# Performance work log

Hardware: AMD Instinct MI355X
Metric: run time of the kernel (lower is better)

## Reference

```python
import jax, jax.numpy as jnp
import numpy as np

N = 100000   # nodes
E = 1600000  # edges
D = 128      # in_dim == hidden_dim (residual-friendly)
C = 47       # num_classes
EPS = 1e-5   # BatchNorm eps


def _glorot(key, shape):
    fan = shape[0] + shape[1]
    return jax.random.uniform(key, shape, jnp.float32, -1.0, 1.0) * np.sqrt(6.0 / fan)


def setup_inputs() -> dict:
    key = jax.random.key(0)
    ks = jax.random.split(key, 16)
    inp = {
        "x": jax.random.normal(ks[0], (N, D), jnp.float32),
        "edge_index": jax.random.randint(ks[1], (2, E), 0, N, jnp.int32),
    }
    # Per-layer SAGEConv params: lin_l (root, with bias) and lin_r (neighbor, no bias)
    for i, k in zip((1, 2, 3), (ks[2], ks[3], ks[4])):
        k1, k2 = jax.random.split(k)
        inp[f"Wl{i}"] = _glorot(k1, (D, D))
        inp[f"bl{i}"] = jnp.zeros((D,), jnp.float32)
        inp[f"Wr{i}"] = _glorot(k2, (D, D))
        inp[f"bn_g{i}"] = jnp.ones((D,), jnp.float32)
        inp[f"bn_b{i}"] = jnp.zeros((D,), jnp.float32)
    inp["lin_W"] = _glorot(ks[5], (C, D))
    inp["lin_b"] = jnp.zeros((C,), jnp.float32)
    return inp


def _sage_conv(x, src, dst, Wl, bl, Wr):
    # mean aggregation of source features at destination nodes
    msg = jax.ops.segment_sum(x[src], dst, num_segments=N)            # [N, D]
    cnt = jax.ops.segment_sum(jnp.ones((src.shape[0],), x.dtype), dst, num_segments=N)
    mean = msg / jnp.maximum(cnt, 1.0)[:, None]
    return x @ Wl.T + bl + mean @ Wr.T


def _batch_norm(h, g, b):
    mu = h.mean(axis=0)
    var = h.var(axis=0)
    return (h - mu) * jax.lax.rsqrt(var + EPS) * g + b


def reference(x, edge_index,
              Wl1, bl1, Wr1, bn_g1, bn_b1,
              Wl2, bl2, Wr2, bn_g2, bn_b2,
              Wl3, bl3, Wr3, bn_g3, bn_b3,
              lin_W, lin_b):
    src, dst = edge_index[0], edge_index[1]
    layers = [(Wl1, bl1, Wr1, bn_g1, bn_b1),
              (Wl2, bl2, Wr2, bn_g2, bn_b2),
              (Wl3, bl3, Wr3, bn_g3, bn_b3)]
    for Wl, bl, Wr, g, b in layers:
        h = _sage_conv(x, src, dst, Wl, bl, Wr)
        h = jax.nn.relu(_batch_norm(h, g, b))
        # dropout is identity in deterministic/eval reference
        x = x + h  # shapes always match since in_dim == hidden_dim
    return x @ lin_W.T + lin_b
```

## Files before the change

kernel.cpp:

```cpp
#include <hip/hip_runtime.h>

typedef __attribute__((ext_vector_type(8))) short short8;
typedef __attribute__((ext_vector_type(4))) float f32x4;
typedef __attribute__((ext_vector_type(2))) float f32x2;

constexpr int NN = 100000;
constexpr int EE = 1600000;
constexpr int DD = 128;
constexpr int CC = 47;
constexpr int NB = 391;
constexpr int BSLOT = 5120;
constexpr int GB = 782;

constexpr size_t OFF_XB   = 0;
constexpr size_t OFF_MB   = 25600000;
constexpr size_t OFF_HB   = 51200000;
constexpr size_t OFF_XQ   = 76800000;
constexpr size_t OFF_BIN  = 89600000;
constexpr size_t OFF_CSR  = 97607680;
constexpr size_t OFF_RP   = 104007680;
constexpr size_t OFF_CUR  = 104407808;
constexpr size_t OFF_BASE = 104409856;
constexpr size_t OFF_W    = 104411904;
constexpr size_t OFF_ST   = 104620800;
constexpr size_t OFF_PB   = 104621824;

static __device__ __forceinline__ float bf2f(unsigned short u) {
    return __uint_as_float(((unsigned)u) << 16);
}
static __device__ __forceinline__ unsigned short f2bf(float f) {
    unsigned u = __float_as_uint(f);
    unsigned r = (u + 0x7fffu + ((u >> 16) & 1u)) >> 16;
    return (unsigned short)r;
}
static __device__ __forceinline__ uint2 pack8_fp8(const float* f) {
    int w0 = 0, w1 = 0;
    w0 = __builtin_amdgcn_cvt_pk_fp8_f32(f[0], f[1], w0, false);
    w0 = __builtin_amdgcn_cvt_pk_fp8_f32(f[2], f[3], w0, true);
    w1 = __builtin_amdgcn_cvt_pk_fp8_f32(f[4], f[5], w1, false);
    w1 = __builtin_amdgcn_cvt_pk_fp8_f32(f[6], f[7], w1, true);
    return uint2{(unsigned)w0, (unsigned)w1};
}

__global__ void k_convw(const float* __restrict__ wl1, const float* __restrict__ wr1,
                        const float* __restrict__ wl2, const float* __restrict__ wr2,
                        const float* __restrict__ wl3, const float* __restrict__ wr3,
                        const float* __restrict__ lw, unsigned short* __restrict__ dst) {
    int id = blockIdx.x * 256 + threadIdx.x;
    if (id < 98304) {
        int L = id >> 15;
        int r = id & 32767;
        int mat = r >> 14;
        int t = r & 16383;
        int j = t & 7, lane = (t >> 3) & 63, ct = (t >> 9) & 7, ks = t >> 12;
        int row = ct * 16 + (lane & 15);
        int col = ks * 32 + ((lane >> 4) << 3) + j;
        const float* src = (L == 0) ? (mat ? wr1 : wl1)
                         : (L == 1) ? (mat ? wr2 : wl2)
                                    : (mat ? wr3 : wl3);
        dst[id] = f2bf(src[row * 128 + col]);
    } else if (id < 98304 + 6144) {
        int t = id - 98304;
        int j = t & 7, lane = (t >> 3) & 63, m = t >> 9;
        int ct = m % 3, ks = m / 3;
        int row = ct * 16 + (lane & 15);
        int col = ks * 32 + ((lane >> 4) << 3) + j;
        dst[id] = (row < CC) ? f2bf(lw[row * 128 + col]) : (unsigned short)0;
    }
}

__global__ void k_convx(const float* __restrict__ x, unsigned short* __restrict__ xb,
                        unsigned char* __restrict__ xq) {
    int i = (blockIdx.x * 256 + threadIdx.x) * 8;
    if (i >= NN * DD) return;
    float4 v1 = *(const float4*)(x + i);
    float4 v2 = *(const float4*)(x + i + 4);
    float f[8] = {v1.x, v1.y, v1.z, v1.w, v2.x, v2.y, v2.z, v2.w};
    short8 o;
    #pragma unroll
    for (int j = 0; j < 8; ++j) o[j] = (short)f2bf(f[j]);
    *(short8*)(xb + i) = o;
    *(uint2*)(xq + i) = pack8_fp8(f);
}

__global__ __launch_bounds__(256) void k_bin(const int* __restrict__ ei,
                                             int* __restrict__ cur, int* __restrict__ bin) {
    __shared__ int cnt[NB];
    int t = threadIdx.x;
    for (int b = t; b < NB; b += 256) cnt[b] = 0;
    __syncthreads();
    int start = blockIdx.x * 3125;
    for (int i = t; i < 3125; i += 256) {
        int d = ei[EE + start + i];
        atomicAdd(&cnt[d >> 8], 1);
    }
    __syncthreads();
    int c[2], b0[2];
    #pragma unroll
    for (int k = 0; k < 2; ++k) {
        int b = t + k * 256;
        if (b < NB) { c[k] = cnt[b]; b0[k] = (c[k] > 0) ? atomicAdd(&cur[b], c[k]) : 0; }
    }
    __syncthreads();
    #pragma unroll
    for (int k = 0; k < 2; ++k) {
        int b = t + k * 256;
        if (b < NB) cnt[b] = b0[k];
    }
    __syncthreads();
    for (int i = t; i < 3125; i += 256) {
        int s = ei[start + i];
        int d = ei[EE + start + i];
        int b = d >> 8;
        int p = atomicAdd(&cnt[b], 1);
        if (p < BSLOT) bin[b * BSLOT + p] = (s << 8) | (d & 255);
    }
}

__global__ void k_base(const int* __restrict__ cur, int* __restrict__ base, int* __restrict__ rp) {
    __shared__ int sd[512];
    int t = threadIdx.x;
    int v0 = (t < NB) ? cur[t] : 0;
    sd[t] = v0;
    __syncthreads();
    for (int off = 1; off < 512; off <<= 1) {
        int v = (t >= off) ? sd[t - off] : 0;
        __syncthreads();
        sd[t] += v;
        __syncthreads();
    }
    if (t < NB) base[t] = sd[t] - v0;
    if (t == NB - 1) rp[NN] = sd[t];
}

__global__ __launch_bounds__(256) void k_build(const int* __restrict__ cur, const int* __restrict__ base,
                                               int* __restrict__ rp, const int* __restrict__ bin,
                                               int* __restrict__ csr) {
    __shared__ int lcnt[256], lsc[256], lrun[256];
    int b = blockIdx.x, t = threadIdx.x;
    int n0 = b << 8;
    int nodes = NN - n0; if (nodes > 256) nodes = 256;
    int tot = cur[b]; if (tot > BSLOT) tot = BSLOT;
    int bb = base[b];
    lcnt[t] = 0;
    __syncthreads();
    const int* bsrc = bin + b * BSLOT;
    for (int i = t; i < tot; i += 256) atomicAdd(&lcnt[bsrc[i] & 255], 1);
    __syncthreads();
    int c = lcnt[t];
    lsc[t] = c;
    __syncthreads();
    for (int off = 1; off < 256; off <<= 1) {
        int v = (t >= off) ? lsc[t - off] : 0;
        __syncthreads();
        lsc[t] += v;
        __syncthreads();
    }
    int excl = lsc[t] - c;
    if (t < nodes) rp[n0 + t] = bb + excl;
    lrun[t] = bb + excl;
    __syncthreads();
    for (int i = t; i < tot; i += 256) {
        int v = bsrc[i];
        int p = atomicAdd(&lrun[v & 255], 1);
        csr[p] = v >> 8;
    }
}

__global__ __launch_bounds__(256) void k_agg(const int* __restrict__ rp, const int* __restrict__ csr,
                                             const unsigned char* __restrict__ xq,
                                             unsigned short* __restrict__ mb) {
    int node = blockIdx.x * 4 + (threadIdx.x >> 6);
    if (node >= NN) return;
    int lane = threadIdx.x & 63;
    int g = lane >> 4;
    int cb = (lane & 15) << 3;
    int s0 = rp[node], s1 = rp[node + 1];
    float acc[8] = {0.f,0.f,0.f,0.f,0.f,0.f,0.f,0.f};
    int e = s0 + g;
    int nx = (e < s1) ? csr[e] : 0;
    for (; e < s1; e += 4) {
        int cur = nx;
        if (e + 4 < s1) nx = csr[e + 4];
        uint2 v = *(const uint2*)(xq + (size_t)cur * 128 + cb);
        f32x2 p0 = __builtin_amdgcn_cvt_pk_f32_fp8(v.x, false);
        f32x2 p1 = __builtin_amdgcn_cvt_pk_f32_fp8(v.x, true);
        f32x2 p2 = __builtin_amdgcn_cvt_pk_f32_fp8(v.y, false);
        f32x2 p3 = __builtin_amdgcn_cvt_pk_f32_fp8(v.y, true);
        acc[0] += p0[0]; acc[1] += p0[1];
        acc[2] += p1[0]; acc[3] += p1[1];
        acc[4] += p2[0]; acc[5] += p2[1];
        acc[6] += p3[0]; acc[7] += p3[1];
    }
    #pragma unroll
    for (int j = 0; j < 8; ++j) {
        acc[j] += __shfl_xor(acc[j], 16);
        acc[j] += __shfl_xor(acc[j], 32);
    }
    if (g == 0) {
        int deg = s1 - s0;
        float inv = 1.0f / (float)(deg > 1 ? deg : 1);
        short8 o;
        #pragma unroll
        for (int j = 0; j < 8; ++j) o[j] = (short)f2bf(acc[j] * inv);
        *(short8*)(mb + (size_t)node * 128 + cb) = o;
    }
}

__global__ __launch_bounds__(256, 4) void k_gemm(const unsigned short* __restrict__ xb,
                                                 const unsigned short* __restrict__ mb,
                                                 const unsigned short* __restrict__ wf,
                                                 const float* __restrict__ bias,
                                                 unsigned short* __restrict__ hb,
                                                 float* __restrict__ pbuf) {
    __shared__ unsigned short wsh[16384];
    __shared__ float rbuf[1024];
    int tid = threadIdx.x;
    int wave = tid >> 6, lane = tid & 63, q = lane >> 4, l15 = lane & 15;
    int rowbase = blockIdx.x * 128 + wave * 32;

    f32x4 acc[2][8];
    #pragma unroll
    for (int ct = 0; ct < 8; ++ct) {
        float bv = bias[ct * 16 + l15];
        f32x4 t = {bv, bv, bv, bv};
        acc[0][ct] = t; acc[1][ct] = t;
    }

    #pragma unroll
    for (int mat = 0; mat < 2; ++mat) {
        const unsigned short* src = mat ? mb : xb;
        const int4* wsrc = (const int4*)(wf + (mat << 14));
        if (mat) __syncthreads();
        #pragma unroll
        for (int i = 0; i < 8; ++i)
            ((int4*)wsh)[tid + i * 256] = wsrc[tid + i * 256];
        __syncthreads();
        #pragma unroll
        for (int ks = 0; ks < 4; ++ks) {
            short8 a[2];
            #pragma unroll
            for (int rt = 0; rt < 2; ++rt) {
                int row = rowbase + rt * 16 + l15;
                if (row < NN) a[rt] = *(const short8*)(src + (size_t)row * 128 + ks * 32 + (q << 3));
                else          a[rt] = short8{0,0,0,0,0,0,0,0};
            }
            #pragma unroll
            for (int ct = 0; ct < 8; ++ct) {
                short8 b = *(const short8*)(wsh + ((ks * 8 + ct) << 9) + (lane << 3));
                acc[0][ct] = __builtin_amdgcn_mfma_f32_16x16x32_bf16(a[0], b, acc[0][ct], 0, 0, 0);
                acc[1][ct] = __builtin_amdgcn_mfma_f32_16x16x32_bf16(a[1], b, acc[1][ct], 0, 0, 0);
            }
        }
    }

    #pragma unroll
    for (int ct = 0; ct < 8; ++ct) {
        int colg = ct * 16 + l15;
        float sv = 0.f, qv = 0.f;
        #pragma unroll
        for (int rt = 0; rt < 2; ++rt) {
            #pragma unroll
            for (int r = 0; r < 4; ++r) {
                int row = rowbase + rt * 16 + (q << 2) + r;
                if (row < NN) {
                    float v = acc[rt][ct][r];
                    hb[(size_t)row * 128 + colg] = f2bf(v);
                    sv += v; qv += v * v;
                }
            }
        }
        sv += __shfl_xor(sv, 16); sv += __shfl_xor(sv, 32);
        qv += __shfl_xor(qv, 16); qv += __shfl_xor(qv, 32);
        if (q == 0) {
            rbuf[wave * 256 + colg] = sv;
            rbuf[wave * 256 + 128 + colg] = qv;
        }
    }
    __syncthreads();
    if (tid < 256) {
        float v = rbuf[tid] + rbuf[256 + tid] + rbuf[512 + tid] + rbuf[768 + tid];
        pbuf[(size_t)blockIdx.x * 256 + tid] = v;
    }
}

__global__ void k_stat2(const float* __restrict__ pbuf, float* __restrict__ st) {
    int b = blockIdx.x, t = threadIdx.x;
    int r0 = b * 98;
    int r1 = r0 + 98; if (r1 > GB) r1 = GB;
    float s = 0.f;
    for (int r = r0; r < r1; ++r) s += pbuf[(size_t)r * 256 + t];
    atomicAdd(&st[t], s);
}

__global__ void k_bn(const unsigned short* __restrict__ hb,
                     const float* __restrict__ stats, const float* __restrict__ gam,
                     const float* __restrict__ bet, unsigned short* __restrict__ xb,
                     unsigned char* __restrict__ xq) {
    int i = (blockIdx.x * 256 + threadIdx.x) * 8;
    if (i >= NN * DD) return;
    int col = i & 127;
    const float invN = 1.0f / (float)NN;
    short8 hv = *(const short8*)(hb + i);
    short8 xv = *(const short8*)(xb + i);
    short8 o;
    float f[8];
    #pragma unroll
    for (int j = 0; j < 8; ++j) {
        int c = col + j;
        float mu = stats[c] * invN;
        float var = stats[128 + c] * invN - mu * mu;
        float sc = rsqrtf(var + 1e-5f) * gam[c];
        float val = (bf2f((unsigned short)hv[j]) - mu) * sc + bet[c];
        float r = bf2f((unsigned short)xv[j]) + (val > 0.f ? val : 0.f);
        f[j] = r;
        o[j] = (short)f2bf(r);
    }
    *(short8*)(xb + i) = o;
    *(uint2*)(xq + i) = pack8_fp8(f);
}

__global__ __launch_bounds__(256) void k_final(const unsigned short* __restrict__ xb,
                                               const unsigned short* __restrict__ wf,
                                               const float* __restrict__ bias,
                                               float* __restrict__ out) {
    __shared__ unsigned short wsh[6144];
    int tid = threadIdx.x;
    #pragma unroll
    for (int i = 0; i < 3; ++i) {
        int idx = tid + i * 256;
        if (idx < 768) ((int4*)wsh)[idx] = ((const int4*)wf)[idx];
    }
    __syncthreads();

    int wave = tid >> 6, lane = tid & 63, q = lane >> 4, l15 = lane & 15;
    int rowbase = blockIdx.x * 256 + wave * 64;

    f32x4 acc[4][3];
    #pragma unroll
    for (int ct = 0; ct < 3; ++ct) {
        int colg = ct * 16 + l15;
        float bv = (colg < CC) ? bias[colg] : 0.f;
        f32x4 t = {bv, bv, bv, bv};
        #pragma unroll
        for (int rt = 0; rt < 4; ++rt) acc[rt][ct] = t;
    }
    #pragma unroll
    for (int ks = 0; ks < 4; ++ks) {
        short8 a[4];
        #pragma unroll
        for (int rt = 0; rt < 4; ++rt) {
            int row = rowbase + rt * 16 + l15;
            if (row < NN) a[rt] = *(const short8*)(xb + (size_t)row * 128 + ks * 32 + (q << 3));
            else          a[rt] = short8{0,0,0,0,0,0,0,0};
        }
        #pragma unroll
        for (int ct = 0; ct < 3; ++ct) {
            short8 b = *(const short8*)(wsh + ((ks * 3 + ct) << 9) + (lane << 3));
            #pragma unroll
            for (int rt = 0; rt < 4; ++rt)
                acc[rt][ct] = __builtin_amdgcn_mfma_f32_16x16x32_bf16(a[rt], b, acc[rt][ct], 0, 0, 0);
        }
    }
    #pragma unroll
    for (int ct = 0; ct < 3; ++ct) {
        int colg = ct * 16 + l15;
        if (colg >= CC) continue;
        #pragma unroll
        for (int rt = 0; rt < 4; ++rt) {
            #pragma unroll
            for (int r = 0; r < 4; ++r) {
                int row = rowbase + rt * 16 + (q << 2) + r;
                if (row < NN) out[(size_t)row * CC + colg] = acc[rt][ct][r];
            }
        }
    }
}

extern "C" void kernel_launch(void* const* d_in, const int* in_sizes, int n_in,
                              void* d_out, int out_size, void* d_ws, size_t ws_size,
                              hipStream_t stream) {
    const float* x   = (const float*)d_in[0];
    const int*   ei  = (const int*)d_in[1];
    const float* Wl[3]  = {(const float*)d_in[2],  (const float*)d_in[7],  (const float*)d_in[12]};
    const float* bl[3]  = {(const float*)d_in[3],  (const float*)d_in[8],  (const float*)d_in[13]};
    const float* Wr[3]  = {(const float*)d_in[4],  (const float*)d_in[9],  (const float*)d_in[14]};
    const float* bng[3] = {(const float*)d_in[5],  (const float*)d_in[10], (const float*)d_in[15]};
    const float* bnb[3] = {(const float*)d_in[6],  (const float*)d_in[11], (const float*)d_in[16]};
    const float* linW = (const float*)d_in[17];
    const float* linb = (const float*)d_in[18];

    char* ws = (char*)d_ws;
    unsigned short* xb   = (unsigned short*)(ws + OFF_XB);
    unsigned short* mb   = (unsigned short*)(ws + OFF_MB);
    unsigned short* hb   = (unsigned short*)(ws + OFF_HB);
    unsigned char*  xq   = (unsigned char*)(ws + OFF_XQ);
    int*            bin  = (int*)(ws + OFF_BIN);
    int*            csr  = (int*)(ws + OFF_CSR);
    int*            rp   = (int*)(ws + OFF_RP);
    int*            cur  = (int*)(ws + OFF_CUR);
    int*            base = (int*)(ws + OFF_BASE);
    unsigned short* wfr  = (unsigned short*)(ws + OFF_W);
    float*          st   = (float*)(ws + OFF_ST);
    float*          pbuf = (float*)(ws + OFF_PB);

    hipMemsetAsync(cur, 0, (size_t)NB * 4, stream);
    k_convw<<<408, 256, 0, stream>>>(Wl[0], Wr[0], Wl[1], Wr[1], Wl[2], Wr[2], linW, wfr);
    k_convx<<<6250, 256, 0, stream>>>(x, xb, xq);
    k_bin<<<512, 256, 0, stream>>>(ei, cur, bin);
    k_base<<<1, 512, 0, stream>>>(cur, base, rp);
    k_build<<<NB, 256, 0, stream>>>(cur, base, rp, bin, csr);

    for (int l = 0; l < 3; ++l) {
        hipMemsetAsync(st, 0, 1024, stream);
        k_agg<<<25000, 256, 0, stream>>>(rp, csr, xq, mb);
        k_gemm<<<GB, 256, 0, stream>>>(xb, mb, wfr + (size_t)l * 32768, bl[l], hb, pbuf);
        k_stat2<<<8, 256, 0, stream>>>(pbuf, st);
        k_bn<<<6250, 256, 0, stream>>>(hb, st, bng[l], bnb[l], xb, xq);
    }
    k_final<<<391, 256, 0, stream>>>(xb, wfr + 98304, linb, (float*)d_out);
}
```

Before: 525.7 us.

## Slice fp8 features into 32-column planes and store mean aggregate as fp8

The fp8 copy of node features becomes four column-slice planes of 32 bytes per node, so each aggregation block gathers from only one 3.2 MB plane, which is meant to improve L2 hit rate on the random neighbour gathers. The aggregation grid grows to four blocks per node group, one per slice, with 8 edges in flight per wave and nontemporal index loads. The mean output is now stored in fp8 in the same sliced layout and converted back to bf16 inside the GEMM, halving that intermediate's traffic at the cost of extra precision loss on the aggregated features.

Result: slower. 841.2 us (+60.0%).

```diff
diff --git a/kernel.cpp b/kernel.cpp
--- a/kernel.cpp
+++ b/kernel.cpp
@@ -11,6 +11,7 @@
 constexpr int NB = 391;
 constexpr int BSLOT = 5120;
 constexpr int GB = 782;
+constexpr size_t SL = (size_t)NN * 32;
 
 constexpr size_t OFF_XB   = 0;
 constexpr size_t OFF_MB   = 25600000;
@@ -40,6 +41,18 @@
     w1 = __builtin_amdgcn_cvt_pk_fp8_f32(f[4], f[5], w1, false);
     w1 = __builtin_amdgcn_cvt_pk_fp8_f32(f[6], f[7], w1, true);
     return uint2{(unsigned)w0, (unsigned)w1};
+}
+static __device__ __forceinline__ short8 fp8x8_to_bf16(uint2 v) {
+    f32x2 p0 = __builtin_amdgcn_cvt_pk_f32_fp8(v.x, false);
+    f32x2 p1 = __builtin_amdgcn_cvt_pk_f32_fp8(v.x, true);
+    f32x2 p2 = __builtin_amdgcn_cvt_pk_f32_fp8(v.y, false);
+    f32x2 p3 = __builtin_amdgcn_cvt_pk_f32_fp8(v.y, true);
+    short8 o;
+    o[0] = (short)f2bf(p0[0]); o[1] = (short)f2bf(p0[1]);
+    o[2] = (short)f2bf(p1[0]); o[3] = (short)f2bf(p1[1]);
+    o[4] = (short)f2bf(p2[0]); o[5] = (short)f2bf(p2[1]);
+    o[6] = (short)f2bf(p3[0]); o[7] = (short)f2bf(p3[1]);
+    return o;
 }
 
 __global__ void k_convw(const float* __restrict__ wl1, const float* __restrict__ wr1,
@@ -80,7 +93,9 @@
     #pragma unroll
     for (int j = 0; j < 8; ++j) o[j] = (short)f2bf(f[j]);
     *(short8*)(xb + i) = o;
-    *(uint2*)(xq + i) = pack8_fp8(f);
+    int node = i >> 7, col = i & 127;
+    int s = col >> 5, c32 = col & 31;
+    *(uint2*)(xq + (size_t)s * SL + ((size_t)node << 5) + c32) = pack8_fp8(f);
 }
 
 __global__ __launch_bounds__(256) void k_bin(const int* __restrict__ ei,
@@ -169,46 +184,44 @@
 
 __global__ __launch_bounds__(256) void k_agg(const int* __restrict__ rp, const int* __restrict__ csr,
                                              const unsigned char* __restrict__ xq,
-                                             unsigned short* __restrict__ mb) {
-    int node = blockIdx.x * 4 + (threadIdx.x >> 6);
+                                             unsigned char* __restrict__ mb) {
+    int slice = blockIdx.x & 3;
+    int node = (blockIdx.x >> 2) * 4 + (threadIdx.x >> 6);
     if (node >= NN) return;
     int lane = threadIdx.x & 63;
-    int g = lane >> 4;
-    int cb = (lane & 15) << 3;
-    int s0 = rp[node], s1 = rp[node + 1];
-    float acc[8] = {0.f,0.f,0.f,0.f,0.f,0.f,0.f,0.f};
-    int e = s0 + g;
-    int nx = (e < s1) ? csr[e] : 0;
-    for (; e < s1; e += 4) {
-        int cur = nx;
-        if (e + 4 < s1) nx = csr[e + 4];
-        uint2 v = *(const uint2*)(xq + (size_t)cur * 128 + cb);
-        f32x2 p0 = __builtin_amdgcn_cvt_pk_f32_fp8(v.x, false);
-        f32x2 p1 = __builtin_amdgcn_cvt_pk_f32_fp8(v.x, true);
-        f32x2 p2 = __builtin_amdgcn_cvt_pk_f32_fp8(v.y, false);
-        f32x2 p3 = __builtin_amdgcn_cvt_pk_f32_fp8(v.y, true);
-        acc[0] += p0[0]; acc[1] += p0[1];
-        acc[2] += p1[0]; acc[3] += p1[1];
-        acc[4] += p2[0]; acc[5] += p2[1];
-        acc[6] += p3[0]; acc[7] += p3[1];
-    }
-    #pragma unroll
-    for (int j = 0; j < 8; ++j) {
-        acc[j] += __shfl_xor(acc[j], 16);
-        acc[j] += __shfl_xor(acc[j], 32);
-    }
-    if (g == 0) {
+    int slot = lane >> 3;
+    int cw = (lane & 7) << 2;
+    int s0 = __builtin_nontemporal_load(rp + node);
+    int s1 = __builtin_nontemporal_load(rp + node + 1);
+    const unsigned char* xs = xq + (size_t)slice * SL + cw;
+    float a0 = 0.f, a1 = 0.f, a2 = 0.f, a3 = 0.f;
+    for (int e = s0 + slot; e < s1; e += 8) {
+        int src = __builtin_nontemporal_load(csr + e);
+        unsigned v = *(const unsigned*)(xs + ((size_t)src << 5));
+        f32x2 p0 = __builtin_amdgcn_cvt_pk_f32_fp8(v, false);
+        f32x2 p1 = __builtin_amdgcn_cvt_pk_f32_fp8(v, true);
+        a0 += p0[0]; a1 += p0[1]; a2 += p1[0]; a3 += p1[1];
+    }
+    #pragma unroll
+    for (int off = 8; off < 64; off <<= 1) {
+        a0 += __shfl_xor(a0, off);
+        a1 += __shfl_xor(a1, off);
+        a2 += __shfl_xor(a2, off);
+        a3 += __shfl_xor(a3, off);
+    }
+    if (slot == 0) {
         int deg = s1 - s0;
         float inv = 1.0f / (float)(deg > 1 ? deg : 1);
-        short8 o;
-        #pragma unroll
-        for (int j = 0; j < 8; ++j) o[j] = (short)f2bf(acc[j] * inv);
-        *(short8*)(mb + (size_t)node * 128 + cb) = o;
+        int w = 0;
+        w = __builtin_amdgcn_cvt_pk_fp8_f32(a0 * inv, a1 * inv, w, false);
+        w = __builtin_amdgcn_cvt_pk_fp8_f32(a2 * inv, a3 * inv, w, true);
+        __builtin_nontemporal_store((unsigned)w,
+            (unsigned*)(mb + (size_t)slice * SL + ((size_t)node << 5) + cw));
     }
 }
 
 __global__ __launch_bounds__(256, 4) void k_gemm(const unsigned short* __restrict__ xb,
-                                                 const unsigned short* __restrict__ mb,
+                                                 const unsigned char* __restrict__ mb,
                                                  const unsigned short* __restrict__ wf,
                                                  const float* __restrict__ bias,
                                                  unsigned short* __restrict__ hb,
@@ -229,7 +242,6 @@
 
     #pragma unroll
     for (int mat = 0; mat < 2; ++mat) {
-        const unsigned short* src = mat ? mb : xb;
         const int4* wsrc = (const int4*)(wf + (mat << 14));
         if (mat) __syncthreads();
         #pragma unroll
@@ -242,8 +254,13 @@
             #pragma unroll
             for (int rt = 0; rt < 2; ++rt) {
                 int row = rowbase + rt * 16 + l15;
-                if (row < NN) a[rt] = *(const short8*)(src + (size_t)row * 128 + ks * 32 + (q << 3));
-                else          a[rt] = short8{0,0,0,0,0,0,0,0};
+                if (row >= NN) { a[rt] = short8{0,0,0,0,0,0,0,0}; continue; }
+                if (mat == 0) {
+                    a[rt] = *(const short8*)(xb + (size_t)row * 128 + ks * 32 + (q << 3));
+                } else {
+                    uint2 v = *(const uint2*)(mb + (size_t)ks * SL + ((size_t)row << 5) + (q << 3));
+                    a[rt] = fp8x8_to_bf16(v);
+                }
             }
             #pragma unroll
             for (int ct = 0; ct < 8; ++ct) {
@@ -317,7 +334,9 @@
         o[j] = (short)f2bf(r);
     }
     *(short8*)(xb + i) = o;
-    *(uint2*)(xq + i) = pack8_fp8(f);
+    int node = i >> 7;
+    int s = col >> 5, c32 = col & 31;
+    *(uint2*)(xq + (size_t)s * SL + ((size_t)node << 5) + c32) = pack8_fp8(f);
 }
 
 __global__ __launch_bounds__(256) void k_final(const unsigned short* __restrict__ xb,
@@ -392,7 +411,7 @@
 
     char* ws = (char*)d_ws;
     unsigned short* xb   = (unsigned short*)(ws + OFF_XB);
-    unsigned short* mb   = (unsigned short*)(ws + OFF_MB);
+    unsigned char*  mbq  = (unsigned char*)(ws + OFF_MB);
     unsigned short* hb   = (unsigned short*)(ws + OFF_HB);
     unsigned char*  xq   = (unsigned char*)(ws + OFF_XQ);
     int*            bin  = (int*)(ws + OFF_BIN);
@@ -413,8 +432,8 @@
 
     for (int l = 0; l < 3; ++l) {
         hipMemsetAsync(st, 0, 1024, stream);
-        k_agg<<<25000, 256, 0, stream>>>(rp, csr, xq, mb);
-        k_gemm<<<GB, 256, 0, stream>>>(xb, mb, wfr + (size_t)l * 32768, bl[l], hb, pbuf);
+        k_agg<<<100000, 256, 0, stream>>>(rp, csr, xq, mbq);
+        k_gemm<<<GB, 256, 0, stream>>>(xb, mbq, wfr + (size_t)l * 32768, bl[l], hb, pbuf);
         k_stat2<<<8, 256, 0, stream>>>(pbuf, st);
         k_bn<<<6250, 256, 0, stream>>>(hb, st, bng[l], bnb[l], xb, xq);
     }
```
